# Kernel tuning notes

Measured on AMD Instinct MI355X. Metric: run time of the kernel, lower is better.

## Reference

```python
import jax, jax.numpy as jnp
import numpy as np

THRESHOLD = 0.1  # init kwarg threshold
N_HITS_PER_EVENT = 200000
N_EVENTS = 64


def setup_inputs() -> dict:
    key = jax.random.key(0)
    n = N_HITS_PER_EVENT * N_EVENTS
    score = jax.random.uniform(key, (n, 1), dtype=jnp.float32)  # noise score in (0,1)
    row_splits = (jnp.arange(N_EVENTS + 1, dtype=jnp.int32) * N_HITS_PER_EVENT)
    return {"score": score, "row_splits": row_splits}


def reference(score, row_splits):
    """Faithful, fully vectorized version of select_threshold_with_backgather.

    Per segment: keep all vertices with score > threshold PLUS all vertices tied
    with the segment minimum score; non-kept vertices backgather to the FIRST
    kept minimum-score vertex of their segment (new/compacted indexing).
    Returns (sel [M,1], newrs [n_seg+1], backgather [N,1]) in the layer's
    call-output order (sel, newrs, allbackgather).
    """
    s = score[:, 0]
    n = s.shape[0]
    n_seg = row_splits.shape[0] - 1

    # segment id of every vertex from the row splits
    segids = jnp.searchsorted(row_splits, jnp.arange(n, dtype=row_splits.dtype), side='right') - 1
    segids = segids.astype(jnp.int32)

    # per-segment minimum score; ties with the min are all kept (== original isminscore)
    segmin = jax.ops.segment_min(s, segids, num_segments=n_seg)
    ismin = s == segmin[segids]
    keep = (s > THRESHOLD) | ismin

    # global compacted position of each kept vertex (n_previous_rs + local keeprange)
    kept_pos = jnp.cumsum(keep.astype(jnp.int32)) - 1

    # representative = first kept min-score vertex per segment (original minidx + n_previous_rs)
    big = jnp.int32(n)
    rep_pos = jax.ops.segment_min(jnp.where(keep & ismin, kept_pos, big), segids, num_segments=n_seg)

    backgather = jnp.where(keep, kept_pos, rep_pos[segids])

    # selection indices (data-dependent size; computed on concrete values, not under jit)
    sel = jnp.nonzero(keep)[0].astype(jnp.int32)

    counts = jax.ops.segment_sum(keep.astype(jnp.int32), segids, num_segments=n_seg)
    newrs = jnp.concatenate([jnp.zeros((1,), jnp.int32), jnp.cumsum(counts).astype(jnp.int32)])

    return sel[:, None], newrs, backgather[:, None].astype(jnp.int32)
```

## Files before the change

### kernel.cpp

```cpp
#include <hip/hip_runtime.h>
#include <stdint.h>

#define BLOCK 256
#define ITEMS 8
#define TILE (BLOCK * ITEMS)
#define WPB (TILE / 64)
#define MAXSEG 64
#define THRESH 0.1f

typedef unsigned long long u64;

__device__ __forceinline__ int find_seg(const int* rs, int n_seg, int i) {
    int lo = 0, hi = n_seg;
    while (hi - lo > 1) {
        int mid = (lo + hi) >> 1;
        if (rs[mid] <= i) lo = mid; else hi = mid;
    }
    return lo;
}

__global__ __launch_bounds__(BLOCK) void k_min(const float* __restrict__ score,
        const int* __restrict__ row_splits, int n_seg, int n,
        u64* __restrict__ partial_val, int* __restrict__ partial_seg) {
    __shared__ int rs[MAXSEG + 1];
    __shared__ u64 wval[8];
    __shared__ int wseg[8];
    for (int j = threadIdx.x; j <= n_seg; j += BLOCK) rs[j] = row_splits[j];
    __syncthreads();
    int lane = threadIdx.x & 63, wv = threadIdx.x >> 6;
    int wbase = blockIdx.x * TILE + wv * (64 * ITEMS);
    u64 m0 = ~0ull, m1 = ~0ull;
    int sf = 0, sl = 0;
    if (wbase < n) {
        int wend = min(n, wbase + 64 * ITEMS) - 1;
        sf = find_seg(rs, n_seg, wbase);
        sl = find_seg(rs, n_seg, wend);
        int tbase = wbase + lane * ITEMS;
        if (tbase < n) {
            float v[ITEMS];
            if (tbase + ITEMS <= n) {
                float4 f0 = *(const float4*)(score + tbase);
                float4 f1 = *(const float4*)(score + tbase + 4);
                v[0]=f0.x; v[1]=f0.y; v[2]=f0.z; v[3]=f0.w;
                v[4]=f1.x; v[5]=f1.y; v[6]=f1.z; v[7]=f1.w;
            } else {
                for (int j = 0; j < ITEMS; j++) v[j] = (tbase + j < n) ? score[tbase + j] : 1.0f;
            }
            int seg = sf;
            #pragma unroll
            for (int j = 0; j < ITEMS; j++) {
                int i = tbase + j;
                if (i >= n) break;
                while (seg < sl && rs[seg + 1] <= i) seg++;
                u64 p = ((u64)__float_as_uint(v[j]) << 32) | (unsigned int)i;
                if (seg == sf) m0 = min(m0, p); else m1 = min(m1, p);
            }
        }
        for (int o = 32; o > 0; o >>= 1) {
            m0 = min(m0, (u64)__shfl_down((unsigned long long)m0, o, 64));
            m1 = min(m1, (u64)__shfl_down((unsigned long long)m1, o, 64));
        }
    }
    if (lane == 0) {
        wval[2 * wv] = m0;     wseg[2 * wv] = sf;
        wval[2 * wv + 1] = m1; wseg[2 * wv + 1] = (sl != sf) ? sl : -1;
    }
    __syncthreads();
    if (threadIdx.x == 0) {
        int base = blockIdx.x * TILE;
        int endi = min(n, base + TILE) - 1;
        int s0 = find_seg(rs, n_seg, base);
        int s1 = find_seg(rs, n_seg, endi);
        u64 o0 = ~0ull, o1 = ~0ull;
        for (int k = 0; k < 8; k++) {
            if (wseg[k] == s0) o0 = min(o0, wval[k]);
            else if (wseg[k] == s1) o1 = min(o1, wval[k]);
        }
        partial_val[2 * blockIdx.x] = o0;
        partial_seg[2 * blockIdx.x] = s0;
        partial_val[2 * blockIdx.x + 1] = o1;
        partial_seg[2 * blockIdx.x + 1] = (s1 != s0) ? s1 : -1;
    }
}

__global__ __launch_bounds__(BLOCK) void k_reduce(const int* __restrict__ row_splits,
        int n_seg, int n,
        const u64* __restrict__ partial_val, const int* __restrict__ partial_seg,
        u64* __restrict__ seg_packed) {
    int lane = threadIdx.x & 63, wv = threadIdx.x >> 6;
    int s = blockIdx.x * (BLOCK / 64) + wv;
    if (s >= n_seg) return;
    int lo = row_splits[s], hi = row_splits[s + 1];
    u64 m = ~0ull;
    if (hi > lo) {
        int b0 = lo / TILE, b1 = (hi - 1) / TILE;
        for (int e = 2 * b0 + lane; e <= 2 * b1 + 1; e += 64) {
            if (partial_seg[e] == s) m = min(m, partial_val[e]);
        }
    }
    for (int o = 32; o > 0; o >>= 1)
        m = min(m, (u64)__shfl_down((unsigned long long)m, o, 64));
    if (lane == 0) seg_packed[s] = m;
}

__global__ __launch_bounds__(BLOCK) void k_count(const float* __restrict__ score,
        const int* __restrict__ row_splits, int n_seg, int n,
        const u64* __restrict__ seg_packed,
        u64* __restrict__ bitmask, int* __restrict__ block_counts) {
    __shared__ int rs[MAXSEG + 1];
    __shared__ unsigned int smin[MAXSEG];
    __shared__ int wsum[BLOCK / 64];
    for (int j = threadIdx.x; j <= n_seg; j += BLOCK) rs[j] = row_splits[j];
    for (int j = threadIdx.x; j < n_seg; j += BLOCK) smin[j] = (unsigned int)(seg_packed[j] >> 32);
    __syncthreads();
    int lane = threadIdx.x & 63, wv = threadIdx.x >> 6;
    int wbase = blockIdx.x * TILE + wv * 512;
    int nwords = (n + 63) >> 6;
    u64 myword = 0;
    int cnt = 0;
    #pragma unroll
    for (int it = 0; it < 8; it++) {
        int i = wbase + it * 64 + lane;
        bool keep = false;
        if (i < n) {
            float v = score[i];
            int seg = find_seg(rs, n_seg, i);
            keep = (v > THRESH) || (__float_as_uint(v) == smin[seg]);
        }
        u64 bal = __ballot(keep);
        if (lane == it) myword = bal;
        cnt += __popcll(bal);
    }
    if (lane < 8) {
        int w = (wbase >> 6) + lane;
        if (w < nwords) bitmask[w] = myword;
    }
    if (lane == 0) wsum[wv] = cnt;
    __syncthreads();
    if (threadIdx.x == 0)
        block_counts[blockIdx.x] = wsum[0] + wsum[1] + wsum[2] + wsum[3];
}

__global__ __launch_bounds__(BLOCK) void k_scan(const int* __restrict__ counts,
                                                int* __restrict__ offsets, int nb) {
    __shared__ int wtot[BLOCK / 64];
    int per = (nb + BLOCK - 1) / BLOCK;
    int s = per * threadIdx.x, e = min(nb, s + per);
    int sum = 0;
    for (int i = s; i < e; i++) sum += counts[i];
    int lane = threadIdx.x & 63, wv = threadIdx.x >> 6;
    int incl = sum;
    for (int o = 1; o < 64; o <<= 1) {
        int t = __shfl_up(incl, o, 64);
        if (lane >= o) incl += t;
    }
    if (lane == 63) wtot[wv] = incl;
    __syncthreads();
    int excl = incl - sum;
    for (int k = 0; k < wv; k++) excl += wtot[k];
    for (int i = s; i < e; i++) { offsets[i] = excl; excl += counts[i]; }
}

__global__ __launch_bounds__(BLOCK) void k_query(const int* __restrict__ row_splits,
        int n_seg, int n, int M,
        const u64* __restrict__ seg_packed, const u64* __restrict__ bitmask,
        const int* __restrict__ block_offsets,
        int* __restrict__ rep_pos, int* __restrict__ newrs_out) {
    int lane = threadIdx.x & 63, wv = threadIdx.x >> 6;
    int q = blockIdx.x * (BLOCK / 64) + wv;
    int nq = 2 * n_seg + 1;
    if (q >= nq) return;
    unsigned int uidx;
    if (q <= n_seg) uidx = (unsigned int)row_splits[q];
    else uidx = (unsigned int)(seg_packed[q - (n_seg + 1)] & 0xFFFFFFFFu);
    int result;
    if (uidx >= (unsigned int)n) {
        result = M;
    } else {
        int idx = (int)uidx;
        int b = idx / TILE;
        int w0 = b * WPB;
        int wq = idx >> 6;
        int cnt = 0;
        for (int w = w0 + lane; w < wq; w += 64) cnt += __popcll(bitmask[w]);
        if (lane == 0 && (idx & 63)) cnt += __popcll(bitmask[wq] & ((1ull << (idx & 63)) - 1));
        for (int o = 32; o > 0; o >>= 1) cnt += __shfl_down(cnt, o, 64);
        result = block_offsets[b] + cnt;
    }
    if (lane == 0) {
        if (q <= n_seg) newrs_out[q] = result;
        else rep_pos[q - (n_seg + 1)] = result;
    }
}

__global__ __launch_bounds__(BLOCK) void k_output(const int* __restrict__ row_splits,
        int n_seg, int n,
        const int* __restrict__ rep_pos, const u64* __restrict__ bitmask,
        const int* __restrict__ block_offsets,
        int* __restrict__ sel_out, int* __restrict__ back_out) {
    __shared__ int rs[MAXSEG + 1];
    __shared__ int srep[MAXSEG];
    __shared__ u64 swords[WPB];
    __shared__ int wpre[WPB];
    for (int j = threadIdx.x; j <= n_seg; j += BLOCK) rs[j] = row_splits[j];
    for (int j = threadIdx.x; j < n_seg; j += BLOCK) srep[j] = rep_pos[j];
    int base = blockIdx.x * TILE;
    int nw = min(WPB, (n - base + 63) >> 6);
    for (int j = threadIdx.x; j < nw; j += BLOCK) swords[j] = bitmask[(base >> 6) + j];
    __syncthreads();
    if (threadIdx.x == 0) {
        int acc = 0;
        for (int k = 0; k < nw; k++) { wpre[k] = acc; acc += __popcll(swords[k]); }
    }
    __syncthreads();
    int bo = block_offsets[blockIdx.x];
    int lane = threadIdx.x & 63, wv = threadIdx.x >> 6;
    #pragma unroll
    for (int it = 0; it < 8; it++) {
        int widx = wv * 8 + it;
        int i = base + widx * 64 + lane;
        if (i < n) {
            u64 word = swords[widx];
            bool keep = (word >> lane) & 1;
            int val;
            if (keep) {
                int pos = bo + wpre[widx] + __popcll(word & ((1ull << lane) - 1));
                val = pos;
                sel_out[pos] = i;
            } else {
                int seg = find_seg(rs, n_seg, i);
                val = srep[seg];
            }
            back_out[i] = val;
        }
    }
}

extern "C" void kernel_launch(void* const* d_in, const int* in_sizes, int n_in,
                              void* d_out, int out_size, void* d_ws, size_t ws_size,
                              hipStream_t stream) {
    const float* score = (const float*)d_in[0];
    const int* row_splits = (const int*)d_in[1];
    int n = in_sizes[0];
    int n_seg = in_sizes[1] - 1;
    int M = out_size - (n_seg + 1) - n;
    int nb = (n + TILE - 1) / TILE;
    int nwords = (n + 63) / 64;
    (void)nwords;

    u64* seg_packed   = (u64*)d_ws;
    u64* partial_val  = seg_packed + 64;
    int* partial_seg  = (int*)(partial_val + 2 * nb);
    int* rep_pos      = partial_seg + 2 * nb;
    int* block_counts = rep_pos + 64;
    int* block_offsets= block_counts + nb;
    uintptr_t bm_addr = (uintptr_t)(block_offsets + nb);
    bm_addr = (bm_addr + 7) & ~(uintptr_t)7;
    u64* bitmask      = (u64*)bm_addr;

    int* out = (int*)d_out;
    int* sel_out   = out;
    int* newrs_out = out + M;
    int* back_out  = out + M + (n_seg + 1);

    hipLaunchKernelGGL(k_min, dim3(nb), dim3(BLOCK), 0, stream,
                       score, row_splits, n_seg, n, partial_val, partial_seg);
    int rblocks = (n_seg + (BLOCK / 64) - 1) / (BLOCK / 64);
    hipLaunchKernelGGL(k_reduce, dim3(rblocks), dim3(BLOCK), 0, stream,
                       row_splits, n_seg, n, partial_val, partial_seg, seg_packed);
    hipLaunchKernelGGL(k_count, dim3(nb), dim3(BLOCK), 0, stream,
                       score, row_splits, n_seg, n, seg_packed, bitmask, block_counts);
    hipLaunchKernelGGL(k_scan, dim3(1), dim3(BLOCK), 0, stream,
                       block_counts, block_offsets, nb);
    int nq = 2 * n_seg + 1;
    int qblocks = (nq + (BLOCK / 64) - 1) / (BLOCK / 64);
    hipLaunchKernelGGL(k_query, dim3(qblocks), dim3(BLOCK), 0, stream,
                       row_splits, n_seg, n, M, seg_packed, bitmask,
                       block_offsets, rep_pos, newrs_out);
    hipLaunchKernelGGL(k_output, dim3(nb), dim3(BLOCK), 0, stream,
                       row_splits, n_seg, n, rep_pos, bitmask,
                       block_offsets, sel_out, back_out);
}
```

Baseline: 197.2 us.

## Fuse min, threshold bitmask and counts into one pass with min-tie patch-up

```diff
diff --git a/kernel.cpp b/kernel.cpp
--- a/kernel.cpp
+++ b/kernel.cpp
@@ -19,51 +19,52 @@
     return lo;
 }
 
-__global__ __launch_bounds__(BLOCK) void k_min(const float* __restrict__ score,
-        const int* __restrict__ row_splits, int n_seg, int n,
-        u64* __restrict__ partial_val, int* __restrict__ partial_seg) {
+__global__ __launch_bounds__(BLOCK) void k_pass1(const float* __restrict__ score,
+        const int* __restrict__ row_splits, int n_seg, int n, int nwords,
+        u64* __restrict__ partial_val, int* __restrict__ partial_seg,
+        u64* __restrict__ bitmask, int* __restrict__ block_counts) {
     __shared__ int rs[MAXSEG + 1];
     __shared__ u64 wval[8];
     __shared__ int wseg[8];
+    __shared__ int wsum[4];
     for (int j = threadIdx.x; j <= n_seg; j += BLOCK) rs[j] = row_splits[j];
     __syncthreads();
     int lane = threadIdx.x & 63, wv = threadIdx.x >> 6;
-    int wbase = blockIdx.x * TILE + wv * (64 * ITEMS);
-    u64 m0 = ~0ull, m1 = ~0ull;
-    int sf = 0, sl = 0;
+    int wbase = blockIdx.x * TILE + wv * 512;
+    u64 m0 = ~0ull, m1 = ~0ull, myword = 0;
+    int sf = -1, sl = -1, cnt = 0;
     if (wbase < n) {
-        int wend = min(n, wbase + 64 * ITEMS) - 1;
+        int wend = min(n, wbase + 512) - 1;
         sf = find_seg(rs, n_seg, wbase);
         sl = find_seg(rs, n_seg, wend);
-        int tbase = wbase + lane * ITEMS;
-        if (tbase < n) {
-            float v[ITEMS];
-            if (tbase + ITEMS <= n) {
-                float4 f0 = *(const float4*)(score + tbase);
-                float4 f1 = *(const float4*)(score + tbase + 4);
-                v[0]=f0.x; v[1]=f0.y; v[2]=f0.z; v[3]=f0.w;
-                v[4]=f1.x; v[5]=f1.y; v[6]=f1.z; v[7]=f1.w;
-            } else {
-                for (int j = 0; j < ITEMS; j++) v[j] = (tbase + j < n) ? score[tbase + j] : 1.0f;
+        int bval = (sl != sf) ? rs[sf + 1] : 0x7FFFFFFF;
+        #pragma unroll
+        for (int it = 0; it < 8; it++) {
+            int i = wbase + it * 64 + lane;
+            bool keep = false;
+            if (i < n) {
+                float v = score[i];
+                u64 p = ((u64)__float_as_uint(v) << 32) | (unsigned int)i;
+                if (i < bval) m0 = min(m0, p); else m1 = min(m1, p);
+                keep = v > THRESH;
             }
-            int seg = sf;
-            #pragma unroll
-            for (int j = 0; j < ITEMS; j++) {
-                int i = tbase + j;
-                if (i >= n) break;
-                while (seg < sl && rs[seg + 1] <= i) seg++;
-                u64 p = ((u64)__float_as_uint(v[j]) << 32) | (unsigned int)i;
-                if (seg == sf) m0 = min(m0, p); else m1 = min(m1, p);
-            }
+            u64 bal = __ballot(keep);
+            if (lane == it) myword = bal;
+            cnt += __popcll(bal);
         }
         for (int o = 32; o > 0; o >>= 1) {
             m0 = min(m0, (u64)__shfl_down((unsigned long long)m0, o, 64));
             m1 = min(m1, (u64)__shfl_down((unsigned long long)m1, o, 64));
         }
+        if (lane < 8) {
+            int w = (wbase >> 6) + lane;
+            if (w < nwords) bitmask[w] = myword;
+        }
     }
     if (lane == 0) {
         wval[2 * wv] = m0;     wseg[2 * wv] = sf;
         wval[2 * wv + 1] = m1; wseg[2 * wv + 1] = (sl != sf) ? sl : -1;
+        wsum[wv] = cnt;
     }
     __syncthreads();
     if (threadIdx.x == 0) {
@@ -80,116 +81,110 @@
         partial_seg[2 * blockIdx.x] = s0;
         partial_val[2 * blockIdx.x + 1] = o1;
         partial_seg[2 * blockIdx.x + 1] = (s1 != s0) ? s1 : -1;
-    }
-}
-
-__global__ __launch_bounds__(BLOCK) void k_reduce(const int* __restrict__ row_splits,
-        int n_seg, int n,
+        block_counts[blockIdx.x] = wsum[0] + wsum[1] + wsum[2] + wsum[3];
+    }
+}
+
+__global__ __launch_bounds__(BLOCK) void k_mid(const float* __restrict__ score,
+        const int* __restrict__ row_splits, int n_seg, int n, int nb, int M,
         const u64* __restrict__ partial_val, const int* __restrict__ partial_seg,
-        u64* __restrict__ seg_packed) {
+        u64* __restrict__ bitmask, int* __restrict__ block_counts,
+        int* __restrict__ block_offsets,
+        int* __restrict__ rep_pos, int* __restrict__ newrs_out) {
+    __shared__ int rs[MAXSEG + 1];
+    __shared__ u64 segp[MAXSEG];
+    __shared__ int wtot[4];
+    for (int j = threadIdx.x; j <= n_seg; j += BLOCK) rs[j] = row_splits[j];
+    __syncthreads();
     int lane = threadIdx.x & 63, wv = threadIdx.x >> 6;
-    int s = blockIdx.x * (BLOCK / 64) + wv;
-    if (s >= n_seg) return;
-    int lo = row_splits[s], hi = row_splits[s + 1];
-    u64 m = ~0ull;
-    if (hi > lo) {
-        int b0 = lo / TILE, b1 = (hi - 1) / TILE;
-        for (int e = 2 * b0 + lane; e <= 2 * b1 + 1; e += 64) {
-            if (partial_seg[e] == s) m = min(m, partial_val[e]);
-        }
-    }
-    for (int o = 32; o > 0; o >>= 1)
-        m = min(m, (u64)__shfl_down((unsigned long long)m, o, 64));
-    if (lane == 0) seg_packed[s] = m;
-}
-
-__global__ __launch_bounds__(BLOCK) void k_count(const float* __restrict__ score,
-        const int* __restrict__ row_splits, int n_seg, int n,
-        const u64* __restrict__ seg_packed,
-        u64* __restrict__ bitmask, int* __restrict__ block_counts) {
-    __shared__ int rs[MAXSEG + 1];
-    __shared__ unsigned int smin[MAXSEG];
-    __shared__ int wsum[BLOCK / 64];
-    for (int j = threadIdx.x; j <= n_seg; j += BLOCK) rs[j] = row_splits[j];
-    for (int j = threadIdx.x; j < n_seg; j += BLOCK) smin[j] = (unsigned int)(seg_packed[j] >> 32);
-    __syncthreads();
-    int lane = threadIdx.x & 63, wv = threadIdx.x >> 6;
-    int wbase = blockIdx.x * TILE + wv * 512;
-    int nwords = (n + 63) >> 6;
-    u64 myword = 0;
-    int cnt = 0;
-    #pragma unroll
-    for (int it = 0; it < 8; it++) {
-        int i = wbase + it * 64 + lane;
-        bool keep = false;
-        if (i < n) {
-            float v = score[i];
-            int seg = find_seg(rs, n_seg, i);
-            keep = (v > THRESH) || (__float_as_uint(v) == smin[seg]);
-        }
-        u64 bal = __ballot(keep);
-        if (lane == it) myword = bal;
-        cnt += __popcll(bal);
-    }
-    if (lane < 8) {
-        int w = (wbase >> 6) + lane;
-        if (w < nwords) bitmask[w] = myword;
-    }
-    if (lane == 0) wsum[wv] = cnt;
-    __syncthreads();
-    if (threadIdx.x == 0)
-        block_counts[blockIdx.x] = wsum[0] + wsum[1] + wsum[2] + wsum[3];
-}
-
-__global__ __launch_bounds__(BLOCK) void k_scan(const int* __restrict__ counts,
-                                                int* __restrict__ offsets, int nb) {
-    __shared__ int wtot[BLOCK / 64];
-    int per = (nb + BLOCK - 1) / BLOCK;
-    int s = per * threadIdx.x, e = min(nb, s + per);
-    int sum = 0;
-    for (int i = s; i < e; i++) sum += counts[i];
-    int lane = threadIdx.x & 63, wv = threadIdx.x >> 6;
-    int incl = sum;
-    for (int o = 1; o < 64; o <<= 1) {
-        int t = __shfl_up(incl, o, 64);
-        if (lane >= o) incl += t;
-    }
-    if (lane == 63) wtot[wv] = incl;
-    __syncthreads();
-    int excl = incl - sum;
-    for (int k = 0; k < wv; k++) excl += wtot[k];
-    for (int i = s; i < e; i++) { offsets[i] = excl; excl += counts[i]; }
-}
-
-__global__ __launch_bounds__(BLOCK) void k_query(const int* __restrict__ row_splits,
-        int n_seg, int n, int M,
-        const u64* __restrict__ seg_packed, const u64* __restrict__ bitmask,
-        const int* __restrict__ block_offsets,
-        int* __restrict__ rep_pos, int* __restrict__ newrs_out) {
-    int lane = threadIdx.x & 63, wv = threadIdx.x >> 6;
-    int q = blockIdx.x * (BLOCK / 64) + wv;
+
+    for (int s = wv; s < n_seg; s += 4) {
+        int lo = rs[s], hi = rs[s + 1];
+        u64 m = ~0ull;
+        if (hi > lo) {
+            int e0 = 2 * (lo / TILE), e1 = 2 * ((hi - 1) / TILE) + 1;
+            for (int e = e0 + lane; e <= e1; e += 64)
+                if (partial_seg[e] == s) m = min(m, partial_val[e]);
+        }
+        for (int o = 32; o > 0; o >>= 1)
+            m = min(m, (u64)__shfl_down((unsigned long long)m, o, 64));
+        if (lane == 0) segp[s] = m;
+    }
+    __syncthreads();
+
+    for (int s = wv; s < n_seg; s += 4) {
+        u64 sp = segp[s];
+        if (sp == ~0ull) continue;
+        unsigned int smb = (unsigned int)(sp >> 32);
+        if (__uint_as_float(smb) > THRESH) continue;
+        int lo = rs[s], hi = rs[s + 1];
+        int e0 = 2 * (lo / TILE), e1 = 2 * ((hi - 1) / TILE) + 1;
+        for (int eb = e0; eb <= e1; eb += 64) {
+            int e = eb + lane;
+            bool match = (e <= e1) && (partial_seg[e] == s) &&
+                         ((unsigned int)(partial_val[e] >> 32) == smb);
+            u64 mask = __ballot(match);
+            while (mask) {
+                int j = __ffsll((unsigned long long)mask) - 1;
+                mask &= mask - 1;
+                int b = (eb + j) >> 1;
+                int rlo = max(b * TILE, lo);
+                int rhi = min(min((b + 1) * TILE, n), hi);
+                int newc = 0;
+                for (int i = rlo + lane; i < rhi; i += 64) {
+                    if (__float_as_uint(score[i]) == smb) {
+                        atomicOr(&bitmask[i >> 6], 1ull << (i & 63));
+                        newc++;
+                    }
+                }
+                for (int o = 32; o > 0; o >>= 1) newc += __shfl_down(newc, o, 64);
+                if (lane == 0 && newc) atomicAdd(&block_counts[b], newc);
+            }
+        }
+    }
+    __syncthreads();
+
+    {
+        int per = (nb + BLOCK - 1) / BLOCK;
+        int s0 = per * threadIdx.x, e0 = min(nb, s0 + per);
+        int sum = 0;
+        for (int i = s0; i < e0; i++) sum += block_counts[i];
+        int incl = sum;
+        for (int o = 1; o < 64; o <<= 1) {
+            int t = __shfl_up(incl, o, 64);
+            if (lane >= o) incl += t;
+        }
+        if (lane == 63) wtot[wv] = incl;
+        __syncthreads();
+        int excl = incl - sum;
+        for (int k = 0; k < wv; k++) excl += wtot[k];
+        for (int i = s0; i < e0; i++) { block_offsets[i] = excl; excl += block_counts[i]; }
+    }
+    __syncthreads();
+
     int nq = 2 * n_seg + 1;
-    if (q >= nq) return;
-    unsigned int uidx;
-    if (q <= n_seg) uidx = (unsigned int)row_splits[q];
-    else uidx = (unsigned int)(seg_packed[q - (n_seg + 1)] & 0xFFFFFFFFu);
-    int result;
-    if (uidx >= (unsigned int)n) {
-        result = M;
-    } else {
-        int idx = (int)uidx;
-        int b = idx / TILE;
-        int w0 = b * WPB;
-        int wq = idx >> 6;
-        int cnt = 0;
-        for (int w = w0 + lane; w < wq; w += 64) cnt += __popcll(bitmask[w]);
-        if (lane == 0 && (idx & 63)) cnt += __popcll(bitmask[wq] & ((1ull << (idx & 63)) - 1));
-        for (int o = 32; o > 0; o >>= 1) cnt += __shfl_down(cnt, o, 64);
-        result = block_offsets[b] + cnt;
-    }
-    if (lane == 0) {
-        if (q <= n_seg) newrs_out[q] = result;
-        else rep_pos[q - (n_seg + 1)] = result;
+    for (int q = wv; q < nq; q += 4) {
+        unsigned int uidx;
+        if (q <= n_seg) uidx = (unsigned int)rs[q];
+        else uidx = (unsigned int)(segp[q - (n_seg + 1)] & 0xFFFFFFFFu);
+        int result;
+        if (uidx >= (unsigned int)n) {
+            result = M;
+        } else {
+            int idx = (int)uidx;
+            int b = idx / TILE;
+            int wq = idx >> 6;
+            int cnt = 0;
+            for (int w = b * WPB + lane; w < wq; w += 64) cnt += __popcll(bitmask[w]);
+            if (lane == 0 && (idx & 63))
+                cnt += __popcll(bitmask[wq] & ((1ull << (idx & 63)) - 1));
+            for (int o = 32; o > 0; o >>= 1) cnt += __shfl_down(cnt, o, 64);
+            result = block_offsets[b] + cnt;
+        }
+        if (lane == 0) {
+            if (q <= n_seg) newrs_out[q] = result;
+            else rep_pos[q - (n_seg + 1)] = result;
+        }
     }
 }
 
@@ -246,10 +241,8 @@
     int M = out_size - (n_seg + 1) - n;
     int nb = (n + TILE - 1) / TILE;
     int nwords = (n + 63) / 64;
-    (void)nwords;
-
-    u64* seg_packed   = (u64*)d_ws;
-    u64* partial_val  = seg_packed + 64;
+
+    u64* partial_val  = (u64*)d_ws;
     int* partial_seg  = (int*)(partial_val + 2 * nb);
     int* rep_pos      = partial_seg + 2 * nb;
     int* block_counts = rep_pos + 64;
@@ -263,19 +256,12 @@
     int* newrs_out = out + M;
     int* back_out  = out + M + (n_seg + 1);
 
-    hipLaunchKernelGGL(k_min, dim3(nb), dim3(BLOCK), 0, stream,
-                       score, row_splits, n_seg, n, partial_val, partial_seg);
-    int rblocks = (n_seg + (BLOCK / 64) - 1) / (BLOCK / 64);
-    hipLaunchKernelGGL(k_reduce, dim3(rblocks), dim3(BLOCK), 0, stream,
-                       row_splits, n_seg, n, partial_val, partial_seg, seg_packed);
-    hipLaunchKernelGGL(k_count, dim3(nb), dim3(BLOCK), 0, stream,
-                       score, row_splits, n_seg, n, seg_packed, bitmask, block_counts);
-    hipLaunchKernelGGL(k_scan, dim3(1), dim3(BLOCK), 0, stream,
-                       block_counts, block_offsets, nb);
-    int nq = 2 * n_seg + 1;
-    int qblocks = (nq + (BLOCK / 64) - 1) / (BLOCK / 64);
-    hipLaunchKernelGGL(k_query, dim3(qblocks), dim3(BLOCK), 0, stream,
-                       row_splits, n_seg, n, M, seg_packed, bitmask,
+    hipLaunchKernelGGL(k_pass1, dim3(nb), dim3(BLOCK), 0, stream,
+                       score, row_splits, n_seg, n, nwords,
+                       partial_val, partial_seg, bitmask, block_counts);
+    hipLaunchKernelGGL(k_mid, dim3(1), dim3(BLOCK), 0, stream,
+                       score, row_splits, n_seg, n, nb, M,
+                       partial_val, partial_seg, bitmask, block_counts,
                        block_offsets, rep_pos, newrs_out);
     hipLaunchKernelGGL(k_output, dim3(nb), dim3(BLOCK), 0, stream,
                        row_splits, n_seg, n, rep_pos, bitmask,
```

Result: slower. 427.0 us (+116.6%).
